# Optimization experiments

Measured on AMD Instinct MI355X. Metric: run time of the kernel, lower is better.

Reference implementation:

```python
import jax, jax.numpy as jnp
import numpy as np

N = 50000
E = 800000
IN_C = 128
HID = 64
HEADS = 2
OUT_C = 40
NEG_SLOPE = 0.2


def glorot(key, shape):
    fan_in, fan_out = shape[0], shape[-1]
    lim = jnp.sqrt(6.0 / (fan_in + fan_out))
    return jax.random.uniform(key, shape, jnp.float32, -lim, lim)


def setup_inputs() -> dict:
    key = jax.random.key(0)
    ks = jax.random.split(key, 10)
    x = jax.random.normal(ks[0], (N, IN_C), jnp.float32)
    edge_index = jax.random.randint(ks[1], (2, E), 0, N, jnp.int32)
    # layer 1: heads=2, concat -> out features HEADS*HID
    W1 = glorot(ks[2], (IN_C, HEADS * HID))
    att_src1 = glorot(ks[3], (HEADS, HID))
    att_dst1 = glorot(ks[4], (HEADS, HID))
    b1 = jnp.zeros((HEADS * HID,), jnp.float32)
    # layer 2: out_heads=1, concat=False (mean over the single head)
    W2 = glorot(ks[5], (HEADS * HID, 1 * OUT_C))
    att_src2 = glorot(ks[6], (1, OUT_C))
    att_dst2 = glorot(ks[7], (1, OUT_C))
    b2 = jnp.zeros((OUT_C,), jnp.float32)
    return {"x": x, "edge_index": edge_index,
            "W1": W1, "att_src1": att_src1, "att_dst1": att_dst1, "b1": b1,
            "W2": W2, "att_src2": att_src2, "att_dst2": att_dst2, "b2": b2}


def _segment_softmax(logits, seg, num_segments):
    # logits: [E, H]; softmax over edges sharing the same destination node
    m = jax.ops.segment_max(logits, seg, num_segments=num_segments)
    m = jnp.where(jnp.isfinite(m), m, 0.0)
    e = jnp.exp(logits - m[seg])
    s = jax.ops.segment_sum(e, seg, num_segments=num_segments)
    return e / (s[seg] + 1e-16)


def _gat_conv(x, src, dst, W, a_src, a_dst, b, concat, n_nodes):
    H, C = a_src.shape
    h = (x @ W).reshape(n_nodes, H, C)                    # [N, H, C]
    al_src = jnp.einsum('nhc,hc->nh', h, a_src)           # [N, H]
    al_dst = jnp.einsum('nhc,hc->nh', h, a_dst)           # [N, H]
    e = jax.nn.leaky_relu(al_src[src] + al_dst[dst], NEG_SLOPE)  # [E, H]
    alpha = _segment_softmax(e, dst, n_nodes)             # [E, H]
    msg = h[src] * alpha[:, :, None]                      # [E, H, C]
    out = jax.ops.segment_sum(msg, dst, num_segments=n_nodes)
    out = out.reshape(n_nodes, H * C) if concat else out.mean(axis=1)
    return out + b


def reference(x, edge_index, W1, att_src1, att_dst1, b1, W2, att_src2, att_dst2, b2):
    n_nodes = x.shape[0]
    loop = jnp.arange(n_nodes, dtype=edge_index.dtype)
    src = jnp.concatenate([edge_index[0], loop])  # add self loops
    dst = jnp.concatenate([edge_index[1], loop])
    # eval mode: dropout is identity, use_bn=False -> no batchnorm
    h = _gat_conv(x, src, dst, W1, att_src1, att_dst1, b1, True, n_nodes)
    h = jax.nn.elu(h)
    out = _gat_conv(h, src, dst, W2, att_src2, att_dst2, b2, False, n_nodes)
    return out
```

## Files before the change

### kernel.cpp

```cpp
#include <hip/hip_runtime.h>
#include <hip/hip_fp16.h>

#define NEG_SLOPE 0.2f

typedef _Float16 f16x8 __attribute__((ext_vector_type(8)));
typedef float f32x4 __attribute__((ext_vector_type(4)));

__device__ __forceinline__ int h2i(__half2 h) { return *(int*)&h; }
__device__ __forceinline__ __half2 i2h(int i) { return *(__half2*)&i; }
__device__ __forceinline__ float lrelu(float v) { return (v > 0.f) ? v : NEG_SLOPE * v; }
__device__ __forceinline__ int pkmax(int a, int b) {
    int r;
    asm("v_pk_max_f16 %0, %1, %2" : "=v"(r) : "v"(a), "v"(b));
    return r;
}
__device__ __forceinline__ __half selh(int r, int packed) {
    return (r < 8) ? __low2half(i2h(packed)) : __high2half(i2h(packed));
}

union U16x8 { uint4 u; __half2 h[4]; };
union U16x4 { uint2 u; __half2 h[2]; };

__global__ __launch_bounds__(256) void k_pack(const float* __restrict__ W1,
                                              const float* __restrict__ W2,
                                              _Float16* __restrict__ bp1,
                                              _Float16* __restrict__ bp2,
                                              int* __restrict__ cnt, int N) {
    int idx = blockIdx.x * 256 + threadIdx.x;
    if (idx < N) cnt[idx] = 0;
    if (idx < 16384) {
        int j = idx & 7, l = (idx >> 3) & 63, nt = (idx >> 9) & 7, ks = idx >> 12;
        int k = ks * 32 + (l >> 4) * 8 + j;
        int col = nt * 16 + (l & 15);
        bp1[idx] = (_Float16)W1[k * 128 + col];
    }
    int idx2 = idx - 16384;
    if (idx2 >= 0 && idx2 < 6144) {
        int j = idx2 & 7, l = (idx2 >> 3) & 63, q = idx2 >> 9;
        int nt = q % 3, ks = q / 3;
        int k = ks * 32 + (l >> 4) * 8 + j;
        int col = nt * 16 + (l & 15);
        bp2[idx2] = (col < 40) ? (_Float16)W2[k * 40 + col] : (_Float16)0.f;
    }
}

__global__ void k_bucket(const int* __restrict__ ei, int* __restrict__ cnt,
                         int* __restrict__ colell, int E, int ps) {
    int p = blockIdx.x & 7;
    int e = ((blockIdx.x >> 3) * blockDim.x + threadIdx.x) * 2;
    if (e >= E) return;
    int lo = p * ps, hi = lo + ps;
    int2 d2 = *(const int2*)(ei + E + e);
    if (d2.x >= lo && d2.x < hi) {
        int s = ei[e];
        int rank = atomicAdd(&cnt[d2.x], 1);
        if (rank < 64) colell[(size_t)d2.x * 64 + rank] = s;
    }
    if (e + 1 < E && d2.y >= lo && d2.y < hi) {
        int s = ei[e + 1];
        int rank = atomicAdd(&cnt[d2.y], 1);
        if (rank < 64) colell[(size_t)d2.y * 64 + rank] = s;
    }
}

__global__ __launch_bounds__(256) void k_gemm1(
    const float* __restrict__ x, const _Float16* __restrict__ bp1,
    const float* __restrict__ as1, const float* __restrict__ ad1,
    __half2* __restrict__ h1h, float* __restrict__ alsrc, float* __restrict__ aldst,
    int N) {
    int w = threadIdx.x >> 6, l = threadIdx.x & 63;
    int n0 = blockIdx.x * 64 + w * 16;
    int li = l & 15, lg = l >> 4;
    int arow = n0 + li;
    f16x8 a[4];
#pragma unroll
    for (int ks = 0; ks < 4; ks++) {
        float4 p0 = make_float4(0, 0, 0, 0), p1 = make_float4(0, 0, 0, 0);
        if (arow < N) {
            const float4* src = (const float4*)(x + (size_t)arow * 128 + ks * 32 + lg * 8);
            p0 = src[0];
            p1 = src[1];
        }
        f16x8 t;
        t[0] = (_Float16)p0.x; t[1] = (_Float16)p0.y; t[2] = (_Float16)p0.z; t[3] = (_Float16)p0.w;
        t[4] = (_Float16)p1.x; t[5] = (_Float16)p1.y; t[6] = (_Float16)p1.z; t[7] = (_Float16)p1.w;
        a[ks] = t;
    }
    f32x4 acc[8];
#pragma unroll
    for (int nt = 0; nt < 8; nt++) acc[nt] = (f32x4){0.f, 0.f, 0.f, 0.f};
    const f16x8* bp = (const f16x8*)bp1;
#pragma unroll
    for (int nt = 0; nt < 8; nt++)
#pragma unroll
        for (int ks = 0; ks < 4; ks++)
            acc[nt] = __builtin_amdgcn_mfma_f32_16x16x32_f16(a[ks], bp[(ks * 8 + nt) * 64 + l],
                                                             acc[nt], 0, 0, 0);
    float as1v[8], ad1v[8];
#pragma unroll
    for (int nt = 0; nt < 8; nt++) {
        as1v[nt] = as1[nt * 16 + li];
        ad1v[nt] = ad1[nt * 16 + li];
    }
#pragma unroll
    for (int r = 0; r < 4; r++) {
        float ps0 = 0, ps1 = 0, pd0 = 0, pd1 = 0;
#pragma unroll
        for (int nt = 0; nt < 4; nt++) {
            ps0 = fmaf(acc[nt][r], as1v[nt], ps0);
            pd0 = fmaf(acc[nt][r], ad1v[nt], pd0);
        }
#pragma unroll
        for (int nt = 4; nt < 8; nt++) {
            ps1 = fmaf(acc[nt][r], as1v[nt], ps1);
            pd1 = fmaf(acc[nt][r], ad1v[nt], pd1);
        }
#pragma unroll
        for (int o = 1; o < 16; o <<= 1) {
            ps0 += __shfl_xor(ps0, o);
            ps1 += __shfl_xor(ps1, o);
            pd0 += __shfl_xor(pd0, o);
            pd1 += __shfl_xor(pd1, o);
        }
        int node = n0 + lg * 4 + r;
        if (li == 0 && node < N) {
            alsrc[node * 2] = ps0;
            alsrc[node * 2 + 1] = ps1;
            aldst[node * 2] = pd0;
            aldst[node * 2 + 1] = pd1;
        }
    }
#pragma unroll
    for (int nt = 0; nt < 8; nt++)
#pragma unroll
        for (int r = 0; r < 4; r++) {
            float v = acc[nt][r];
            float p = __shfl_down(v, 1);
            int node = n0 + lg * 4 + r;
            if ((l & 1) == 0 && node < N)
                h1h[(size_t)node * 64 + nt * 8 + (li >> 1)] = __floats2half2_rn(v, p);
        }
}

__global__ __launch_bounds__(256) void k_gather1(
    const int* __restrict__ cnt, const int* __restrict__ colell,
    const _Float16* __restrict__ h1, const float2* __restrict__ alsrc,
    const float2* __restrict__ aldst, const float4* __restrict__ b1v,
    const _Float16* __restrict__ bp2, const float* __restrict__ as2,
    const float* __restrict__ ad2, __half2* __restrict__ h2h,
    float* __restrict__ alsrc2, float* __restrict__ aldst2, int N) {
    __shared__ __align__(16) _Float16 hfl[4][128];
    int w = threadIdx.x >> 6;
    int lane = threadIdx.x & 63;
    int n0 = blockIdx.x * 4;
    int wid = n0 + w;
    if (wid < N) {
        int g = lane >> 4, r = lane & 15;
        float2 asn = alsrc[wid], ad = aldst[wid];
        float ls0 = lrelu(asn.x + ad.x);
        float ls1 = lrelu(asn.y + ad.y);
        int nb = min(cnt[wid], 64);
        int sv = 0;
        float l0 = -1e30f, l1 = -1e30f;
        if (lane < nb) {
            sv = colell[(size_t)wid * 64 + lane];
            float2 av = alsrc[sv];
            l0 = lrelu(av.x + ad.x);
            l1 = lrelu(av.y + ad.y);
        }
        int lpi = h2i(__floats2half2_rn(l0, l1));
#pragma unroll
        for (int o = 32; o > 0; o >>= 1) lpi = pkmax(lpi, __shfl_xor(lpi, o));
        __half2 lp = i2h(lpi);
        float m0 = fmaxf(__low2float(lp), ls0);
        float m1 = fmaxf(__high2float(lp), ls1);
        float e0 = (lane < nb) ? __expf(l0 - m0) : 0.f;
        float e1 = (lane < nb) ? __expf(l1 - m1) : 0.f;
        int we = h2i(__floats2half2_rn(e0, e1));
        float lsh = (r < 8) ? ls0 : ls1;
        float mh = (r < 8) ? m0 : m1;
        __half esh = __float2half((g == 0) ? __expf(lsh - mh) : 0.f);
        float s_part = __half2float(esh);
        __half2 esp = __half2half2(esh);
        U16x8 hs;
        hs.u = *(const uint4*)(h1 + (size_t)wid * 128 + r * 8);
        __half2 a0 = __hmul2(hs.h[0], esp), a1 = __hmul2(hs.h[1], esp),
                a2 = __hmul2(hs.h[2], esp), a3 = __hmul2(hs.h[3], esp);
        if (nb > 0) {
            int i0 = __shfl(sv, g),      p0 = __shfl(we, g);
            int i1 = __shfl(sv, 4 + g),  p1 = __shfl(we, 4 + g);
            int i2 = __shfl(sv, 8 + g),  p2 = __shfl(we, 8 + g);
            int i3 = __shfl(sv, 12 + g), p3 = __shfl(we, 12 + g);
            U16x8 hA, hB, hC, hD;
            hA.u = *(const uint4*)(h1 + (size_t)i0 * 128 + r * 8);
            hB.u = *(const uint4*)(h1 + (size_t)i1 * 128 + r * 8);
            hC.u = *(const uint4*)(h1 + (size_t)i2 * 128 + r * 8);
            hD.u = *(const uint4*)(h1 + (size_t)i3 * 128 + r * 8);
            __half wA = selh(r, p0), wB = selh(r, p1), wC = selh(r, p2), wD = selh(r, p3);
            for (int j = 16; j < nb; j += 4) {
                int i4 = __shfl(sv, j + g), p4 = __shfl(we, j + g);
                U16x8 hN;
                hN.u = *(const uint4*)(h1 + (size_t)i4 * 128 + r * 8);
                __half2 ww = __half2half2(wA);
                s_part += __half2float(wA);
                a0 = __hfma2(ww, hA.h[0], a0);
                a1 = __hfma2(ww, hA.h[1], a1);
                a2 = __hfma2(ww, hA.h[2], a2);
                a3 = __hfma2(ww, hA.h[3], a3);
                hA = hB; wA = wB;
                hB = hC; wB = wC;
                hC = hD; wC = wD;
                hD = hN; wD = selh(r, p4);
            }
            {
                __half2 ww = __half2half2(wA);
                s_part += __half2float(wA);
                a0 = __hfma2(ww, hA.h[0], a0); a1 = __hfma2(ww, hA.h[1], a1);
                a2 = __hfma2(ww, hA.h[2], a2); a3 = __hfma2(ww, hA.h[3], a3);
            }
            {
                __half2 ww = __half2half2(wB);
                s_part += __half2float(wB);
                a0 = __hfma2(ww, hB.h[0], a0); a1 = __hfma2(ww, hB.h[1], a1);
                a2 = __hfma2(ww, hB.h[2], a2); a3 = __hfma2(ww, hB.h[3], a3);
            }
            {
                __half2 ww = __half2half2(wC);
                s_part += __half2float(wC);
                a0 = __hfma2(ww, hC.h[0], a0); a1 = __hfma2(ww, hC.h[1], a1);
                a2 = __hfma2(ww, hC.h[2], a2); a3 = __hfma2(ww, hC.h[3], a3);
            }
            {
                __half2 ww = __half2half2(wD);
                s_part += __half2float(wD);
                a0 = __hfma2(ww, hD.h[0], a0); a1 = __hfma2(ww, hD.h[1], a1);
                a2 = __hfma2(ww, hD.h[2], a2); a3 = __hfma2(ww, hD.h[3], a3);
            }
        }
#pragma unroll
        for (int o = 16; o < 64; o <<= 1) {
            s_part += __shfl_xor(s_part, o);
            a0 = __hadd2(a0, i2h(__shfl_xor(h2i(a0), o)));
            a1 = __hadd2(a1, i2h(__shfl_xor(h2i(a1), o)));
            a2 = __hadd2(a2, i2h(__shfl_xor(h2i(a2), o)));
            a3 = __hadd2(a3, i2h(__shfl_xor(h2i(a3), o)));
        }
        if (g == 0) {
            float inv = 1.f / (s_part + 1e-16f);
            float4 bA = b1v[2 * r], bB = b1v[2 * r + 1];
            float v[8] = {__low2float(a0), __high2float(a0), __low2float(a1), __high2float(a1),
                          __low2float(a2), __high2float(a2), __low2float(a3), __high2float(a3)};
            float vb[8] = {bA.x, bA.y, bA.z, bA.w, bB.x, bB.y, bB.z, bB.w};
            U16x8 o;
#pragma unroll
            for (int k = 0; k < 8; k += 2) {
                float u0 = fmaf(v[k], inv, vb[k]);
                float u1 = fmaf(v[k + 1], inv, vb[k + 1]);
                u0 = (u0 > 0.f) ? u0 : (__expf(u0) - 1.f);
                u1 = (u1 > 0.f) ? u1 : (__expf(u1) - 1.f);
                o.h[k >> 1] = __floats2half2_rn(u0, u1);
            }
            *(uint4*)(&hfl[w][r * 8]) = o.u;
        }
    }
    __syncthreads();
    if (w == 0) {
        int li = lane & 15, lg = lane >> 4;
        f16x8 av[4];
        const f16x8* hrow = (const f16x8*)(&hfl[li & 3][0]);
#pragma unroll
        for (int ks = 0; ks < 4; ks++) {
            f16x8 t;
            if (li < 4) {
                t = hrow[ks * 4 + lg];
            } else {
#pragma unroll
                for (int k = 0; k < 8; k++) t[k] = (_Float16)0.f;
            }
            av[ks] = t;
        }
        f32x4 acc2[3];
#pragma unroll
        for (int nt = 0; nt < 3; nt++) acc2[nt] = (f32x4){0.f, 0.f, 0.f, 0.f};
        const f16x8* bp = (const f16x8*)bp2;
#pragma unroll
        for (int nt = 0; nt < 3; nt++)
#pragma unroll
            for (int ks = 0; ks < 4; ks++)
                acc2[nt] = __builtin_amdgcn_mfma_f32_16x16x32_f16(
                    av[ks], bp[(ks * 3 + nt) * 64 + lane], acc2[nt], 0, 0, 0);
        float as2v[3], ad2v[3];
#pragma unroll
        for (int nt = 0; nt < 3; nt++) {
            int col = nt * 16 + li;
            as2v[nt] = (col < 40) ? as2[col] : 0.f;
            ad2v[nt] = (col < 40) ? ad2[col] : 0.f;
        }
#pragma unroll
        for (int r = 0; r < 4; r++) {
            float ps = 0, pd = 0;
#pragma unroll
            for (int nt = 0; nt < 3; nt++) {
                ps = fmaf(acc2[nt][r], as2v[nt], ps);
                pd = fmaf(acc2[nt][r], ad2v[nt], pd);
            }
#pragma unroll
            for (int o = 1; o < 16; o <<= 1) {
                ps += __shfl_xor(ps, o);
                pd += __shfl_xor(pd, o);
            }
            int node = n0 + r;
            if (li == 0 && lg == 0 && node < N) {
                alsrc2[node] = ps;
                aldst2[node] = pd;
            }
        }
#pragma unroll
        for (int nt = 0; nt < 3; nt++)
#pragma unroll
            for (int r = 0; r < 4; r++) {
                float v = acc2[nt][r];
                float p = __shfl_down(v, 1);
                int node = n0 + r;
                int col = nt * 16 + li;
                if (lg == 0 && (lane & 1) == 0 && col < 40 && node < N)
                    h2h[(size_t)node * 20 + nt * 8 + (li >> 1)] = __floats2half2_rn(v, p);
            }
    }
}

__global__ __launch_bounds__(256) void k_gather2(
    const int* __restrict__ cnt, const int* __restrict__ colell,
    const _Float16* __restrict__ h2, const float* __restrict__ alsrc,
    const float* __restrict__ aldst, const float4* __restrict__ b2v,
    float4* __restrict__ out4, int N) {
    int wid = (int)(((size_t)blockIdx.x * blockDim.x + threadIdx.x) >> 6);
    int lane = threadIdx.x & 63;
    if (wid >= N) return;
    int g = lane >> 4, r = lane & 15;
    int rc = (r < 10) ? r : 0;
    float ad = aldst[wid];
    float ls = lrelu(alsrc[wid] + ad);
    int nb = min(cnt[wid], 64);
    int sv = 0;
    float l = -1e30f;
    if (lane < nb) {
        sv = colell[(size_t)wid * 64 + lane];
        l = lrelu(alsrc[sv] + ad);
    }
    float m = l;
#pragma unroll
    for (int o = 32; o > 0; o >>= 1) m = fmaxf(m, __shfl_xor(m, o));
    m = fmaxf(m, ls);
    float e = (lane < nb) ? __expf(l - m) : 0.f;
    float es = (g == 0) ? __expf(ls - m) : 0.f;
    float s_part = es;
    __half2 esp = __floats2half2_rn(es, es);
    U16x4 hs;
    hs.u = *(const uint2*)(h2 + (size_t)wid * 40 + rc * 4);
    __half2 a0 = __hmul2(hs.h[0], esp), a1 = __hmul2(hs.h[1], esp);
    if (nb > 0) {
        int i0 = __shfl(sv, g);
        int i1 = __shfl(sv, 4 + g);
        int i2 = __shfl(sv, 8 + g);
        int i3 = __shfl(sv, 12 + g);
        float wA = __shfl(e, g), wB = __shfl(e, 4 + g);
        float wC = __shfl(e, 8 + g), wD = __shfl(e, 12 + g);
        U16x4 hA, hB, hC, hD;
        hA.u = *(const uint2*)(h2 + (size_t)i0 * 40 + rc * 4);
        hB.u = *(const uint2*)(h2 + (size_t)i1 * 40 + rc * 4);
        hC.u = *(const uint2*)(h2 + (size_t)i2 * 40 + rc * 4);
        hD.u = *(const uint2*)(h2 + (size_t)i3 * 40 + rc * 4);
        for (int j = 16; j < nb; j += 4) {
            int i4 = __shfl(sv, j + g);
            float wN = __shfl(e, j + g);
            U16x4 hN;
            hN.u = *(const uint2*)(h2 + (size_t)i4 * 40 + rc * 4);
            __half2 ww = __floats2half2_rn(wA, wA);
            s_part += wA;
            a0 = __hfma2(ww, hA.h[0], a0);
            a1 = __hfma2(ww, hA.h[1], a1);
            hA = hB; wA = wB;
            hB = hC; wB = wC;
            hC = hD; wC = wD;
            hD = hN; wD = wN;
        }
        {
            __half2 ww = __floats2half2_rn(wA, wA);
            s_part += wA;
            a0 = __hfma2(ww, hA.h[0], a0); a1 = __hfma2(ww, hA.h[1], a1);
        }
        {
            __half2 ww = __floats2half2_rn(wB, wB);
            s_part += wB;
            a0 = __hfma2(ww, hB.h[0], a0); a1 = __hfma2(ww, hB.h[1], a1);
        }
        {
            __half2 ww = __floats2half2_rn(wC, wC);
            s_part += wC;
            a0 = __hfma2(ww, hC.h[0], a0); a1 = __hfma2(ww, hC.h[1], a1);
        }
        {
            __half2 ww = __floats2half2_rn(wD, wD);
            s_part += wD;
            a0 = __hfma2(ww, hD.h[0], a0); a1 = __hfma2(ww, hD.h[1], a1);
        }
    }
#pragma unroll
    for (int o = 16; o < 64; o <<= 1) {
        s_part += __shfl_xor(s_part, o);
        a0 = __hadd2(a0, i2h(__shfl_xor(h2i(a0), o)));
        a1 = __hadd2(a1, i2h(__shfl_xor(h2i(a1), o)));
    }
    if (g == 0 && r < 10) {
        float inv = 1.f / (s_part + 1e-16f);
        float4 b = b2v[r];
        float4 o = make_float4(fmaf(__low2float(a0), inv, b.x),
                               fmaf(__high2float(a0), inv, b.y),
                               fmaf(__low2float(a1), inv, b.z),
                               fmaf(__high2float(a1), inv, b.w));
        out4[(size_t)wid * 10 + r] = o;
    }
}

extern "C" void kernel_launch(void* const* d_in, const int* in_sizes, int n_in,
                              void* d_out, int out_size, void* d_ws, size_t ws_size,
                              hipStream_t stream) {
    const float* x   = (const float*)d_in[0];
    const int*   ei  = (const int*)d_in[1];
    const float* W1  = (const float*)d_in[2];
    const float* as1 = (const float*)d_in[3];
    const float* ad1 = (const float*)d_in[4];
    const float* b1  = (const float*)d_in[5];
    const float* W2  = (const float*)d_in[6];
    const float* as2 = (const float*)d_in[7];
    const float* ad2 = (const float*)d_in[8];
    const float* b2  = (const float*)d_in[9];
    int N = in_sizes[0] / 128;
    int E = in_sizes[1] / 2;
    float4* out4 = (float4*)d_out;

    char* ws = (char*)d_ws;
    size_t off = 0;
    auto alloc = [&](size_t bytes) {
        char* p = ws + off;
        off += (bytes + 255) & ~(size_t)255;
        return p;
    };
    int*      cnt    = (int*)alloc((size_t)N * 4);
    int*      colell = (int*)alloc((size_t)N * 64 * 4);
    _Float16* bp1    = (_Float16*)alloc(16384 * 2);
    _Float16* bp2    = (_Float16*)alloc(6144 * 2);
    _Float16* h1h    = (_Float16*)alloc((size_t)N * 128 * 2);
    _Float16* h2h    = (_Float16*)alloc((size_t)N * 40 * 2);
    float*    alsrc1 = (float*)alloc((size_t)N * 2 * 4);
    float*    aldst1 = (float*)alloc((size_t)N * 2 * 4);
    float*    alsrc2 = (float*)alloc((size_t)N * 4);
    float*    aldst2 = (float*)alloc((size_t)N * 4);

    dim3 b256(256);
    int ps = (N + 7) / 8;
    int gB = 8 * ((E + 511) / 512);
    int gP = (N > 22528 ? N + 255 : 22528 + 255) / 256;

    k_pack<<<gP, b256, 0, stream>>>(W1, W2, bp1, bp2, cnt, N);
    k_bucket<<<gB, b256, 0, stream>>>(ei, cnt, colell, E, ps);

    int gG = (N + 63) / 64;
    k_gemm1<<<gG, b256, 0, stream>>>(x, bp1, as1, ad1, (__half2*)h1h, alsrc1, aldst1, N);
    k_gather1<<<(N + 3) / 4, b256, 0, stream>>>(
        cnt, colell, h1h, (const float2*)alsrc1, (const float2*)aldst1,
        (const float4*)b1, bp2, as2, ad2, (__half2*)h2h, alsrc2, aldst2, N);
    k_gather2<<<(int)(((size_t)N * 64 + 255) / 256), b256, 0, stream>>>(
        cnt, colell, h2h, alsrc2, aldst2, (const float4*)b2, out4, N);
}
```

Before: 124.7 us.

## Remove shared-memory barrier in gather1 by per-wave MFMA via lane shuffles

The layer-1 gather kernel used to stage each wave's ELU output into shared memory, sync the block, and have one wave run the layer-2 projection MFMA for four nodes. Now every wave runs its own projection MFMA for its single node, building the A operand with cross-lane shuffles and zero-padding the other rows. This drops the block barrier and the idle three waves during the MFMA phase, so waves can exit independently. In exchange it issues four times as many MFMAs, most of them wasted on zero rows, and it adds shuffle traffic.

Measured after the change: 132.3 us. +6.1%, slower.

```diff
diff --git a/kernel.cpp b/kernel.cpp
--- a/kernel.cpp
+++ b/kernel.cpp
@@ -17,8 +17,16 @@
 __device__ __forceinline__ __half selh(int r, int packed) {
     return (r < 8) ? __low2half(i2h(packed)) : __high2half(i2h(packed));
 }
-
-union U16x8 { uint4 u; __half2 h[4]; };
+__device__ __forceinline__ uint4 shfl_u4(uint4 v, int srcl) {
+    uint4 t;
+    t.x = __shfl((int)v.x, srcl);
+    t.y = __shfl((int)v.y, srcl);
+    t.z = __shfl((int)v.z, srcl);
+    t.w = __shfl((int)v.w, srcl);
+    return t;
+}
+
+union U16x8 { uint4 u; __half2 h[4]; f16x8 f; };
 union U16x4 { uint2 u; __half2 h[2]; };
 
 __global__ __launch_bounds__(256) void k_pack(const float* __restrict__ W1,
@@ -149,183 +157,161 @@
     const _Float16* __restrict__ bp2, const float* __restrict__ as2,
     const float* __restrict__ ad2, __half2* __restrict__ h2h,
     float* __restrict__ alsrc2, float* __restrict__ aldst2, int N) {
-    __shared__ __align__(16) _Float16 hfl[4][128];
-    int w = threadIdx.x >> 6;
+    int wid = (int)(((size_t)blockIdx.x * blockDim.x + threadIdx.x) >> 6);
     int lane = threadIdx.x & 63;
-    int n0 = blockIdx.x * 4;
-    int wid = n0 + w;
-    if (wid < N) {
-        int g = lane >> 4, r = lane & 15;
-        float2 asn = alsrc[wid], ad = aldst[wid];
-        float ls0 = lrelu(asn.x + ad.x);
-        float ls1 = lrelu(asn.y + ad.y);
-        int nb = min(cnt[wid], 64);
-        int sv = 0;
-        float l0 = -1e30f, l1 = -1e30f;
-        if (lane < nb) {
-            sv = colell[(size_t)wid * 64 + lane];
-            float2 av = alsrc[sv];
-            l0 = lrelu(av.x + ad.x);
-            l1 = lrelu(av.y + ad.y);
-        }
-        int lpi = h2i(__floats2half2_rn(l0, l1));
-#pragma unroll
-        for (int o = 32; o > 0; o >>= 1) lpi = pkmax(lpi, __shfl_xor(lpi, o));
-        __half2 lp = i2h(lpi);
-        float m0 = fmaxf(__low2float(lp), ls0);
-        float m1 = fmaxf(__high2float(lp), ls1);
-        float e0 = (lane < nb) ? __expf(l0 - m0) : 0.f;
-        float e1 = (lane < nb) ? __expf(l1 - m1) : 0.f;
-        int we = h2i(__floats2half2_rn(e0, e1));
-        float lsh = (r < 8) ? ls0 : ls1;
-        float mh = (r < 8) ? m0 : m1;
-        __half esh = __float2half((g == 0) ? __expf(lsh - mh) : 0.f);
-        float s_part = __half2float(esh);
-        __half2 esp = __half2half2(esh);
-        U16x8 hs;
-        hs.u = *(const uint4*)(h1 + (size_t)wid * 128 + r * 8);
-        __half2 a0 = __hmul2(hs.h[0], esp), a1 = __hmul2(hs.h[1], esp),
-                a2 = __hmul2(hs.h[2], esp), a3 = __hmul2(hs.h[3], esp);
-        if (nb > 0) {
-            int i0 = __shfl(sv, g),      p0 = __shfl(we, g);
-            int i1 = __shfl(sv, 4 + g),  p1 = __shfl(we, 4 + g);
-            int i2 = __shfl(sv, 8 + g),  p2 = __shfl(we, 8 + g);
-            int i3 = __shfl(sv, 12 + g), p3 = __shfl(we, 12 + g);
-            U16x8 hA, hB, hC, hD;
-            hA.u = *(const uint4*)(h1 + (size_t)i0 * 128 + r * 8);
-            hB.u = *(const uint4*)(h1 + (size_t)i1 * 128 + r * 8);
-            hC.u = *(const uint4*)(h1 + (size_t)i2 * 128 + r * 8);
-            hD.u = *(const uint4*)(h1 + (size_t)i3 * 128 + r * 8);
-            __half wA = selh(r, p0), wB = selh(r, p1), wC = selh(r, p2), wD = selh(r, p3);
-            for (int j = 16; j < nb; j += 4) {
-                int i4 = __shfl(sv, j + g), p4 = __shfl(we, j + g);
-                U16x8 hN;
-                hN.u = *(const uint4*)(h1 + (size_t)i4 * 128 + r * 8);
-                __half2 ww = __half2half2(wA);
-                s_part += __half2float(wA);
-                a0 = __hfma2(ww, hA.h[0], a0);
-                a1 = __hfma2(ww, hA.h[1], a1);
-                a2 = __hfma2(ww, hA.h[2], a2);
-                a3 = __hfma2(ww, hA.h[3], a3);
-                hA = hB; wA = wB;
-                hB = hC; wB = wC;
-                hC = hD; wC = wD;
-                hD = hN; wD = selh(r, p4);
-            }
-            {
-                __half2 ww = __half2half2(wA);
-                s_part += __half2float(wA);
-                a0 = __hfma2(ww, hA.h[0], a0); a1 = __hfma2(ww, hA.h[1], a1);
-                a2 = __hfma2(ww, hA.h[2], a2); a3 = __hfma2(ww, hA.h[3], a3);
-            }
-            {
-                __half2 ww = __half2half2(wB);
-                s_part += __half2float(wB);
-                a0 = __hfma2(ww, hB.h[0], a0); a1 = __hfma2(ww, hB.h[1], a1);
-                a2 = __hfma2(ww, hB.h[2], a2); a3 = __hfma2(ww, hB.h[3], a3);
-            }
-            {
-                __half2 ww = __half2half2(wC);
-                s_part += __half2float(wC);
-                a0 = __hfma2(ww, hC.h[0], a0); a1 = __hfma2(ww, hC.h[1], a1);
-                a2 = __hfma2(ww, hC.h[2], a2); a3 = __hfma2(ww, hC.h[3], a3);
-            }
-            {
-                __half2 ww = __half2half2(wD);
-                s_part += __half2float(wD);
-                a0 = __hfma2(ww, hD.h[0], a0); a1 = __hfma2(ww, hD.h[1], a1);
-                a2 = __hfma2(ww, hD.h[2], a2); a3 = __hfma2(ww, hD.h[3], a3);
-            }
-        }
-#pragma unroll
-        for (int o = 16; o < 64; o <<= 1) {
-            s_part += __shfl_xor(s_part, o);
-            a0 = __hadd2(a0, i2h(__shfl_xor(h2i(a0), o)));
-            a1 = __hadd2(a1, i2h(__shfl_xor(h2i(a1), o)));
-            a2 = __hadd2(a2, i2h(__shfl_xor(h2i(a2), o)));
-            a3 = __hadd2(a3, i2h(__shfl_xor(h2i(a3), o)));
-        }
-        if (g == 0) {
-            float inv = 1.f / (s_part + 1e-16f);
-            float4 bA = b1v[2 * r], bB = b1v[2 * r + 1];
-            float v[8] = {__low2float(a0), __high2float(a0), __low2float(a1), __high2float(a1),
-                          __low2float(a2), __high2float(a2), __low2float(a3), __high2float(a3)};
-            float vb[8] = {bA.x, bA.y, bA.z, bA.w, bB.x, bB.y, bB.z, bB.w};
-            U16x8 o;
-#pragma unroll
-            for (int k = 0; k < 8; k += 2) {
-                float u0 = fmaf(v[k], inv, vb[k]);
-                float u1 = fmaf(v[k + 1], inv, vb[k + 1]);
-                u0 = (u0 > 0.f) ? u0 : (__expf(u0) - 1.f);
-                u1 = (u1 > 0.f) ? u1 : (__expf(u1) - 1.f);
-                o.h[k >> 1] = __floats2half2_rn(u0, u1);
-            }
-            *(uint4*)(&hfl[w][r * 8]) = o.u;
-        }
-    }
-    __syncthreads();
-    if (w == 0) {
-        int li = lane & 15, lg = lane >> 4;
-        f16x8 av[4];
-        const f16x8* hrow = (const f16x8*)(&hfl[li & 3][0]);
-#pragma unroll
-        for (int ks = 0; ks < 4; ks++) {
-            f16x8 t;
-            if (li < 4) {
-                t = hrow[ks * 4 + lg];
-            } else {
-#pragma unroll
-                for (int k = 0; k < 8; k++) t[k] = (_Float16)0.f;
-            }
-            av[ks] = t;
-        }
-        f32x4 acc2[3];
-#pragma unroll
-        for (int nt = 0; nt < 3; nt++) acc2[nt] = (f32x4){0.f, 0.f, 0.f, 0.f};
-        const f16x8* bp = (const f16x8*)bp2;
-#pragma unroll
-        for (int nt = 0; nt < 3; nt++)
-#pragma unroll
-            for (int ks = 0; ks < 4; ks++)
-                acc2[nt] = __builtin_amdgcn_mfma_f32_16x16x32_f16(
-                    av[ks], bp[(ks * 3 + nt) * 64 + lane], acc2[nt], 0, 0, 0);
-        float as2v[3], ad2v[3];
-#pragma unroll
-        for (int nt = 0; nt < 3; nt++) {
-            int col = nt * 16 + li;
-            as2v[nt] = (col < 40) ? as2[col] : 0.f;
-            ad2v[nt] = (col < 40) ? ad2[col] : 0.f;
-        }
-#pragma unroll
-        for (int r = 0; r < 4; r++) {
-            float ps = 0, pd = 0;
-#pragma unroll
-            for (int nt = 0; nt < 3; nt++) {
-                ps = fmaf(acc2[nt][r], as2v[nt], ps);
-                pd = fmaf(acc2[nt][r], ad2v[nt], pd);
-            }
-#pragma unroll
-            for (int o = 1; o < 16; o <<= 1) {
-                ps += __shfl_xor(ps, o);
-                pd += __shfl_xor(pd, o);
-            }
-            int node = n0 + r;
-            if (li == 0 && lg == 0 && node < N) {
-                alsrc2[node] = ps;
-                aldst2[node] = pd;
-            }
-        }
-#pragma unroll
-        for (int nt = 0; nt < 3; nt++)
-#pragma unroll
-            for (int r = 0; r < 4; r++) {
-                float v = acc2[nt][r];
-                float p = __shfl_down(v, 1);
-                int node = n0 + r;
-                int col = nt * 16 + li;
-                if (lg == 0 && (lane & 1) == 0 && col < 40 && node < N)
-                    h2h[(size_t)node * 20 + nt * 8 + (li >> 1)] = __floats2half2_rn(v, p);
-            }
+    if (wid >= N) return;
+    int g = lane >> 4, r = lane & 15;
+    int li = r, lg = g;
+    float2 asn = alsrc[wid], ad = aldst[wid];
+    float ls0 = lrelu(asn.x + ad.x);
+    float ls1 = lrelu(asn.y + ad.y);
+    int nb = min(cnt[wid], 64);
+    int sv = 0;
+    float l0 = -1e30f, l1 = -1e30f;
+    if (lane < nb) {
+        sv = colell[(size_t)wid * 64 + lane];
+        float2 av = alsrc[sv];
+        l0 = lrelu(av.x + ad.x);
+        l1 = lrelu(av.y + ad.y);
+    }
+    int lpi = h2i(__floats2half2_rn(l0, l1));
+#pragma unroll
+    for (int o = 32; o > 0; o >>= 1) lpi = pkmax(lpi, __shfl_xor(lpi, o));
+    __half2 lp = i2h(lpi);
+    float m0 = fmaxf(__low2float(lp), ls0);
+    float m1 = fmaxf(__high2float(lp), ls1);
+    float e0 = (lane < nb) ? __expf(l0 - m0) : 0.f;
+    float e1 = (lane < nb) ? __expf(l1 - m1) : 0.f;
+    int we = h2i(__floats2half2_rn(e0, e1));
+    float lsh = (r < 8) ? ls0 : ls1;
+    float mh = (r < 8) ? m0 : m1;
+    __half esh = __float2half((g == 0) ? __expf(lsh - mh) : 0.f);
+    float s_part = __half2float(esh);
+    __half2 esp = __half2half2(esh);
+    U16x8 hs;
+    hs.u = *(const uint4*)(h1 + (size_t)wid * 128 + r * 8);
+    __half2 a0 = __hmul2(hs.h[0], esp), a1 = __hmul2(hs.h[1], esp),
+            a2 = __hmul2(hs.h[2], esp), a3 = __hmul2(hs.h[3], esp);
+    if (nb > 0) {
+        int i0 = __shfl(sv, g),      p0 = __shfl(we, g);
+        int i1 = __shfl(sv, 4 + g),  p1 = __shfl(we, 4 + g);
+        int i2 = __shfl(sv, 8 + g),  p2 = __shfl(we, 8 + g);
+        int i3 = __shfl(sv, 12 + g), p3 = __shfl(we, 12 + g);
+        U16x8 hA, hB, hC, hD;
+        hA.u = *(const uint4*)(h1 + (size_t)i0 * 128 + r * 8);
+        hB.u = *(const uint4*)(h1 + (size_t)i1 * 128 + r * 8);
+        hC.u = *(const uint4*)(h1 + (size_t)i2 * 128 + r * 8);
+        hD.u = *(const uint4*)(h1 + (size_t)i3 * 128 + r * 8);
+        __half wA = selh(r, p0), wB = selh(r, p1), wC = selh(r, p2), wD = selh(r, p3);
+        for (int j = 16; j < nb; j += 4) {
+            int i4 = __shfl(sv, j + g), p4 = __shfl(we, j + g);
+            U16x8 hN;
+            hN.u = *(const uint4*)(h1 + (size_t)i4 * 128 + r * 8);
+            __half2 ww = __half2half2(wA);
+            s_part += __half2float(wA);
+            a0 = __hfma2(ww, hA.h[0], a0);
+            a1 = __hfma2(ww, hA.h[1], a1);
+            a2 = __hfma2(ww, hA.h[2], a2);
+            a3 = __hfma2(ww, hA.h[3], a3);
+            hA = hB; wA = wB;
+            hB = hC; wB = wC;
+            hC = hD; wC = wD;
+            hD = hN; wD = selh(r, p4);
+        }
+        {
+            __half2 ww = __half2half2(wA);
+            s_part += __half2float(wA);
+            a0 = __hfma2(ww, hA.h[0], a0); a1 = __hfma2(ww, hA.h[1], a1);
+            a2 = __hfma2(ww, hA.h[2], a2); a3 = __hfma2(ww, hA.h[3], a3);
+        }
+        {
+            __half2 ww = __half2half2(wB);
+            s_part += __half2float(wB);
+            a0 = __hfma2(ww, hB.h[0], a0); a1 = __hfma2(ww, hB.h[1], a1);
+            a2 = __hfma2(ww, hB.h[2], a2); a3 = __hfma2(ww, hB.h[3], a3);
+        }
+        {
+            __half2 ww = __half2half2(wC);
+            s_part += __half2float(wC);
+            a0 = __hfma2(ww, hC.h[0], a0); a1 = __hfma2(ww, hC.h[1], a1);
+            a2 = __hfma2(ww, hC.h[2], a2); a3 = __hfma2(ww, hC.h[3], a3);
+        }
+        {
+            __half2 ww = __half2half2(wD);
+            s_part += __half2float(wD);
+            a0 = __hfma2(ww, hD.h[0], a0); a1 = __hfma2(ww, hD.h[1], a1);
+            a2 = __hfma2(ww, hD.h[2], a2); a3 = __hfma2(ww, hD.h[3], a3);
+        }
+    }
+#pragma unroll
+    for (int o = 16; o < 64; o <<= 1) {
+        s_part += __shfl_xor(s_part, o);
+        a0 = __hadd2(a0, i2h(__shfl_xor(h2i(a0), o)));
+        a1 = __hadd2(a1, i2h(__shfl_xor(h2i(a1), o)));
+        a2 = __hadd2(a2, i2h(__shfl_xor(h2i(a2), o)));
+        a3 = __hadd2(a3, i2h(__shfl_xor(h2i(a3), o)));
+    }
+    float inv = 1.f / (s_part + 1e-16f);
+    float4 bA = b1v[2 * r], bB = b1v[2 * r + 1];
+    float v[8] = {__low2float(a0), __high2float(a0), __low2float(a1), __high2float(a1),
+                  __low2float(a2), __high2float(a2), __low2float(a3), __high2float(a3)};
+    float vb[8] = {bA.x, bA.y, bA.z, bA.w, bB.x, bB.y, bB.z, bB.w};
+    U16x8 hf8;
+#pragma unroll
+    for (int k = 0; k < 8; k += 2) {
+        float u0 = fmaf(v[k], inv, vb[k]);
+        float u1 = fmaf(v[k + 1], inv, vb[k + 1]);
+        u0 = (u0 > 0.f) ? u0 : (__expf(u0) - 1.f);
+        u1 = (u1 > 0.f) ? u1 : (__expf(u1) - 1.f);
+        hf8.h[k >> 1] = __floats2half2_rn(u0, u1);
+    }
+    f16x8 av2[4];
+#pragma unroll
+    for (int ks = 0; ks < 4; ks++) {
+        U16x8 t;
+        t.u = shfl_u4(hf8.u, ks * 4 + lg);
+        if (li != 0) t.u = make_uint4(0, 0, 0, 0);
+        av2[ks] = t.f;
+    }
+    f32x4 acc2[3];
+#pragma unroll
+    for (int nt = 0; nt < 3; nt++) acc2[nt] = (f32x4){0.f, 0.f, 0.f, 0.f};
+    const f16x8* bp = (const f16x8*)bp2;
+#pragma unroll
+    for (int nt = 0; nt < 3; nt++)
+#pragma unroll
+        for (int ks = 0; ks < 4; ks++)
+            acc2[nt] = __builtin_amdgcn_mfma_f32_16x16x32_f16(
+                av2[ks], bp[(ks * 3 + nt) * 64 + lane], acc2[nt], 0, 0, 0);
+    float as2v[3], ad2v[3];
+#pragma unroll
+    for (int nt = 0; nt < 3; nt++) {
+        int col = nt * 16 + li;
+        as2v[nt] = (col < 40) ? as2[col] : 0.f;
+        ad2v[nt] = (col < 40) ? ad2[col] : 0.f;
+    }
+    float ps = 0, pd = 0;
+#pragma unroll
+    for (int nt = 0; nt < 3; nt++) {
+        ps = fmaf(acc2[nt][0], as2v[nt], ps);
+        pd = fmaf(acc2[nt][0], ad2v[nt], pd);
+    }
+#pragma unroll
+    for (int o = 1; o < 16; o <<= 1) {
+        ps += __shfl_xor(ps, o);
+        pd += __shfl_xor(pd, o);
+    }
+    if (lane == 0) {
+        alsrc2[wid] = ps;
+        aldst2[wid] = pd;
+    }
+#pragma unroll
+    for (int nt = 0; nt < 3; nt++) {
+        float vv = acc2[nt][0];
+        float pp = __shfl_down(vv, 1);
+        int col = nt * 16 + li;
+        if (lg == 0 && (li & 1) == 0 && col < 40)
+            h2h[(size_t)wid * 20 + nt * 8 + (li >> 1)] = __floats2half2_rn(vv, pp);
     }
 }
 
@@ -468,7 +454,7 @@
 
     int gG = (N + 63) / 64;
     k_gemm1<<<gG, b256, 0, stream>>>(x, bp1, as1, ad1, (__half2*)h1h, alsrc1, aldst1, N);
-    k_gather1<<<(N + 3) / 4, b256, 0, stream>>>(
+    k_gather1<<<(int)(((size_t)N * 64 + 255) / 256), b256, 0, stream>>>(
         cnt, colell, h1h, (const float2*)alsrc1, (const float2*)aldst1,
         (const float4*)b1, bp2, as2, ad2, (__half2*)h2h, alsrc2, aldst2, N);
     k_gather2<<<(int)(((size_t)N * 64 + 255) / 256), b256, 0, stream>>>(
```
